# Performance work log

Hardware: AMD Instinct MI355X
Metric: run time of the kernel (lower is better)

## Reference

```python
import jax, jax.numpy as jnp
import numpy as np

N = 100000
E = 3200000
F_IN = 27
H1, C1 = 8, 8
H2, C2 = 1, 2
NEG_SLOPE = 0.2


def gat_conv(x, src, dst, W, a_src, a_dst, b, heads, ch, n_nodes):
    # x: [N, F_in]; src/dst: [E'] (self-loops already appended)
    h = (x @ W).reshape(n_nodes, heads, ch)            # [N, H, C]
    alpha_src = jnp.sum(h * a_src, axis=-1)            # [N, H]
    alpha_dst = jnp.sum(h * a_dst, axis=-1)            # [N, H]
    e = jax.nn.leaky_relu(alpha_src[src] + alpha_dst[dst], NEG_SLOPE)  # [E', H]
    m = jax.ops.segment_max(e, dst, num_segments=n_nodes)             # [N, H]
    ex = jnp.exp(e - m[dst])
    denom = jax.ops.segment_sum(ex, dst, num_segments=n_nodes)        # [N, H]
    alpha = ex / denom[dst]                                           # [E', H]
    out = jax.ops.segment_sum(h[src] * alpha[:, :, None], dst, num_segments=n_nodes)
    return out.reshape(n_nodes, heads * ch) + b


def setup_inputs() -> dict:
    key = jax.random.key(0)
    ks = jax.random.split(key, 10)
    x = jax.random.normal(ks[0], (N, F_IN), dtype=jnp.float32)
    edge_index = jax.random.randint(ks[1], (2, E), 0, N, dtype=jnp.int64)
    s1 = 1.0 / np.sqrt(F_IN)
    s2 = 1.0 / np.sqrt(H1 * C1)
    W1 = jax.random.uniform(ks[2], (F_IN, H1 * C1), jnp.float32, -s1, s1)
    a_src1 = jax.random.uniform(ks[3], (H1, C1), jnp.float32, -s1, s1)
    a_dst1 = jax.random.uniform(ks[4], (H1, C1), jnp.float32, -s1, s1)
    b1 = jnp.zeros((H1 * C1,), jnp.float32)
    W2 = jax.random.uniform(ks[5], (H1 * C1, H2 * C2), jnp.float32, -s2, s2)
    a_src2 = jax.random.uniform(ks[6], (H2, C2), jnp.float32, -s2, s2)
    a_dst2 = jax.random.uniform(ks[7], (H2, C2), jnp.float32, -s2, s2)
    b2 = jnp.zeros((H2 * C2,), jnp.float32)
    return {"x": x, "edge_index": edge_index, "W1": W1, "a_src1": a_src1,
            "a_dst1": a_dst1, "b1": b1, "W2": W2, "a_src2": a_src2,
            "a_dst2": a_dst2, "b2": b2}


def reference(x, edge_index, W1, a_src1, a_dst1, b1, W2, a_src2, a_dst2, b2):
    # eval mode: dropouts are identity. PyG GATConv adds self-loops by default.
    loop = jnp.arange(N, dtype=edge_index.dtype)
    src = jnp.concatenate([edge_index[0], loop])
    dst = jnp.concatenate([edge_index[1], loop])
    h = jax.nn.elu(gat_conv(x, src, dst, W1, a_src1, a_dst1, b1, H1, C1, N))
    out = gat_conv(h, src, dst, W2, a_src2, a_dst2, b2, H2, C2, N)
    return jax.nn.log_softmax(out, axis=1)
```

## Files before the change

kernel.cpp:

```cpp
#include <hip/hip_runtime.h>
#include <hip/hip_fp16.h>
#include <math.h>

#define NN 100000
#define EE 3200000
#define ET (EE + NN)

#define H1n 8
#define C1n 8
#define F1n 64
#define FINn 27
#define NEG 0.2f

#define NPB 128
#define NB 782
#define STRIDE 5120
#define TILE 4096
#define ABLK 256
#define WIN (STRIDE + NPB)
#define FBLK 512
#define RPT 10

typedef float floatx2 __attribute__((ext_vector_type(2)));

static __device__ __forceinline__ float lrelu(float v) {
    return v > 0.f ? v : NEG * v;
}

__global__ __launch_bounds__(ABLK) void k_binA(const int* __restrict__ ei,
                                               int* __restrict__ tail,
                                               int* __restrict__ recs) {
    __shared__ int hist[NB];
    __shared__ int lofs[NB];
    __shared__ int gpos[NB];
    __shared__ int sorted[TILE];
    __shared__ unsigned short sbkt[TILE];
    __shared__ int part[ABLK];

    int tid = threadIdx.x;
    long long e0 = (long long)blockIdx.x * TILE;
    int cnt = (int)min((long long)TILE, (long long)EE - e0);

    for (int i = tid; i < NB; i += ABLK) hist[i] = 0;
    __syncthreads();

    int ss[TILE / ABLK], dd[TILE / ABLK], rk[TILE / ABLK];
    #pragma unroll
    for (int k = 0; k < TILE / ABLK; ++k) {
        int idx = k * ABLK + tid;
        if (idx < cnt) {
            ss[k] = ei[e0 + idx];
            dd[k] = ei[EE + e0 + idx];
            rk[k] = atomicAdd(&hist[dd[k] >> 7], 1);
        }
    }
    __syncthreads();
    {
        const int CH = (NB + ABLK - 1) / ABLK;
        int beg = tid * CH, end = min(beg + CH, NB);
        int s = 0;
        for (int i = beg; i < end; ++i) s += hist[i];
        part[tid] = s;
        __syncthreads();
        for (int off = 1; off < ABLK; off <<= 1) {
            int add = (tid >= off) ? part[tid - off] : 0;
            __syncthreads();
            part[tid] += add;
            __syncthreads();
        }
        int ex = (tid > 0) ? part[tid - 1] : 0;
        for (int i = beg; i < end; ++i) {
            lofs[i] = ex;
            ex += hist[i];
        }
    }
    __syncthreads();
    #pragma unroll
    for (int k = 0; k < TILE / ABLK; ++k) {
        int idx = k * ABLK + tid;
        if (idx < cnt) {
            int b = dd[k] >> 7;
            int r = lofs[b] + rk[k];
            sorted[r] = ss[k] | ((dd[k] & (NPB - 1)) << 17);
            sbkt[r] = (unsigned short)b;
        }
    }
    __syncthreads();
    for (int i = tid; i < NB; i += ABLK) {
        int c = hist[i];
        if (c > 0) gpos[i] = atomicAdd(&tail[i], c);
    }
    __syncthreads();
    for (int t = tid; t < cnt; t += ABLK) {
        int b = sbkt[t];
        recs[(size_t)b * STRIDE + gpos[b] + (t - lofs[b])] = sorted[t];
    }
}

__global__ __launch_bounds__(256) void k_h1(const float* __restrict__ x,
                                            const float* __restrict__ W1,
                                            const float* __restrict__ a_src1,
                                            const float* __restrict__ a_dst1,
                                            unsigned char* __restrict__ h1qA,
                                            unsigned char* __restrict__ h1qB,
                                            __half* __restrict__ as1hA,
                                            __half* __restrict__ as1hB,
                                            float* __restrict__ ad1) {
    int gt = blockIdx.x * blockDim.x + threadIdx.x;
    int n = gt >> 6;
    if (n >= NN) return;
    int lane = threadIdx.x & 63;
    const float* xr = x + (size_t)n * FINn;
    float s = 0.f;
    #pragma unroll
    for (int k = 0; k < FINn; ++k) s = fmaf(xr[k], W1[k * F1n + lane], s);
    float s2 = __shfl_down(s, 1, 64);
    if (!(lane & 1)) {
        int pk = __builtin_amdgcn_cvt_pk_fp8_f32(s, s2, 0, false);
        unsigned char* tb = (lane < 32) ? h1qA : h1qB;
        ((unsigned short*)(tb + (size_t)n * 32))[(lane & 31) >> 1] =
            (unsigned short)(pk & 0xFFFF);
    }
    float ps = s * a_src1[lane];
    float pd = s * a_dst1[lane];
    #pragma unroll
    for (int off = 1; off < 8; off <<= 1) {
        ps += __shfl_xor(ps, off, 64);
        pd += __shfl_xor(pd, off, 64);
    }
    if ((lane & 7) == 0) {
        int h = lane >> 3;
        __half* ta = (h < 4) ? as1hA : as1hB;
        ta[n * 4 + (h & 3)] = __float2half(ps);
        ad1[n * H1n + h] = pd;
    }
}

__global__ __launch_bounds__(FBLK) void k_f1(const int* __restrict__ recs,
                                             const int* __restrict__ tail,
                                             const unsigned* __restrict__ h1qA,
                                             const unsigned* __restrict__ h1qB,
                                             const __half* __restrict__ as1hA,
                                             const __half* __restrict__ as1hB,
                                             const float* __restrict__ ad1,
                                             const float* __restrict__ b1,
                                             const float* __restrict__ W2,
                                             const float* __restrict__ a_src2,
                                             const float* __restrict__ a_dst2,
                                             uint2* __restrict__ rec2,
                                             int* __restrict__ gwin,
                                             uint2* __restrict__ nrange) {
    __shared__ int hist[NPB];
    __shared__ int cur[NPB];
    __shared__ int rloc[NPB + 1];
    __shared__ int window[WIN];
    __shared__ int wtot[2];
    __shared__ float2 part2[NPB];

    int b = blockIdx.x;
    int tid = threadIdx.x;
    int node0 = b * NPB;
    int nodes = min(NPB, NN - node0);
    int rcnt = tail[b];
    const int* rb = recs + (size_t)b * STRIDE;

    if (tid < NPB) hist[tid] = 0;
    __syncthreads();
    int rg[RPT];
    int nmine = 0;
    #pragma unroll
    for (int k = 0; k < RPT; ++k) {
        int i = tid + k * FBLK;
        if (i < rcnt) {
            rg[k] = rb[i];
            atomicAdd(&hist[rg[k] >> 17], 1);
            nmine = k + 1;
        }
    }
    __syncthreads();
    int v = 0, inc = 0;
    if (tid < NPB) {
        v = (tid < nodes) ? hist[tid] + 1 : 0;
        inc = v;
        #pragma unroll
        for (int off = 1; off < 64; off <<= 1) {
            int t = __shfl_up(inc, off, 64);
            if ((tid & 63) >= off) inc += t;
        }
        if ((tid & 63) == 63) wtot[tid >> 6] = inc;
    }
    __syncthreads();
    if (tid < NPB) {
        if (tid >= 64) inc += wtot[0];
        int ex = inc - v;
        if (tid < nodes) {
            rloc[tid] = ex;
            cur[tid] = ex + 1;
            window[ex] = node0 + tid;
        }
    }
    if (tid == 0) rloc[nodes] = wtot[0] + wtot[1];
    __syncthreads();
    #pragma unroll
    for (int k = 0; k < RPT; ++k) {
        if (k < nmine) {
            int r = rg[k];
            int p = atomicAdd(&cur[r >> 17], 1);
            window[p] = r & 0x1FFFF;
        }
    }
    __syncthreads();
    {
        int T = rloc[nodes];
        int gbase = b * WIN;
        for (int i = tid; i < T; i += FBLK)
            gwin[gbase + i] = window[i];
        if (tid < nodes) {
            uint2 r;
            r.x = (unsigned)(gbase + rloc[tid]);
            r.y = (unsigned)(gbase + rloc[tid + 1]);
            nrange[node0 + tid] = r;
        }
    }

    int lane = tid & 63;
    int wv = tid >> 6;
    int hh4 = lane & 3;
    int c4h = lane & 7;
    int bps = lane & 60;
    int bpq = (lane >> 3) << 2;
    int bpx = ((lane >> 3) << 4) + ((c4h >> 1) << 2);

    #pragma unroll
    for (int pass = 0; pass < 2; ++pass) {
        const unsigned* h1h = pass ? h1qB : h1qA;
        const __half* as1h = pass ? as1hB : as1hA;
        int ch0 = pass * 32 + c4h * 4;
        float bch0 = b1[ch0 + 0], bch1 = b1[ch0 + 1];
        float bch2 = b1[ch0 + 2], bch3 = b1[ch0 + 3];
        float w2a0 = W2[(ch0 + 0) * 2], w2b0 = W2[(ch0 + 0) * 2 + 1];
        float w2a1 = W2[(ch0 + 1) * 2], w2b1 = W2[(ch0 + 1) * 2 + 1];
        float w2a2 = W2[(ch0 + 2) * 2], w2b2 = W2[(ch0 + 2) * 2 + 1];
        float w2a3 = W2[(ch0 + 3) * 2], w2b3 = W2[(ch0 + 3) * 2 + 1];

        for (int ln = wv; ln < nodes; ln += FBLK / 64) {
            int n = node0 + ln;
            float adh = ad1[(n << 3) + (pass << 2) + hh4];
            int beg = rloc[ln], end = rloc[ln + 1];
            float a0 = 0.f, a1 = 0.f, a2 = 0.f, a3 = 0.f, den = 0.f;

            for (int base = beg; base < end; base += 64) {
                int cnt = min(64, end - base);
                int sidx = (lane < cnt) ? window[base + lane] : 0;
                for (int sb = 0; sb < cnt; sb += 16) {
                    int sb4 = sb << 2;
                    int s_sc = __builtin_amdgcn_ds_bpermute(sb4 + bps, sidx);
                    float A = __half2float(as1h[((unsigned)s_sc << 2) + hh4]);
                    float sc = A + adh;
                    sc = fmaxf(sc, 0.2f * sc);
                    float x = (sb + (lane >> 2) < cnt) ? __expf(sc) : 0.f;
                    den += x;
                    int xi = __float_as_int(x);
                    #pragma unroll
                    for (int jj = 0; jj < 2; ++jj) {
                        int s_a = __builtin_amdgcn_ds_bpermute(
                            sb4 + (jj << 5) + bpq, sidx);
                        int xr_ = __builtin_amdgcn_ds_bpermute((jj << 7) + bpx, xi);
                        float xv = __int_as_float(xr_);
                        unsigned dw = h1h[((unsigned)s_a << 3) + c4h];
                        floatx2 lo = __builtin_amdgcn_cvt_pk_f32_fp8((int)dw, false);
                        floatx2 hi = __builtin_amdgcn_cvt_pk_f32_fp8((int)dw, true);
                        a0 = fmaf(xv, lo.x, a0);
                        a1 = fmaf(xv, lo.y, a1);
                        a2 = fmaf(xv, hi.x, a2);
                        a3 = fmaf(xv, hi.y, a3);
                    }
                }
            }

            den += __shfl_xor(den, 4, 64);
            den += __shfl_xor(den, 8, 64);
            den += __shfl_xor(den, 16, 64);
            den += __shfl_xor(den, 32, 64);
            den = __int_as_float(__builtin_amdgcn_ds_bpermute(
                (c4h >> 1) << 2, __float_as_int(den)));
            #pragma unroll
            for (int off = 8; off < 64; off <<= 1) {
                a0 += __shfl_xor(a0, off, 64);
                a1 += __shfl_xor(a1, off, 64);
                a2 += __shfl_xor(a2, off, 64);
                a3 += __shfl_xor(a3, off, 64);
            }
            float inv = 1.f / den;
            float v0 = a0 * inv + bch0;
            float v1 = a1 * inv + bch1;
            float v2 = a2 * inv + bch2;
            float v3 = a3 * inv + bch3;
            v0 = v0 > 0.f ? v0 : expm1f(v0);
            v1 = v1 > 0.f ? v1 : expm1f(v1);
            v2 = v2 > 0.f ? v2 : expm1f(v2);
            v3 = v3 > 0.f ? v3 : expm1f(v3);
            float p0 = v0 * w2a0 + v1 * w2a1 + v2 * w2a2 + v3 * w2a3;
            float p1 = v0 * w2b0 + v1 * w2b1 + v2 * w2b2 + v3 * w2b3;
            p0 += __shfl_xor(p0, 1, 64);
            p1 += __shfl_xor(p1, 1, 64);
            p0 += __shfl_xor(p0, 2, 64);
            p1 += __shfl_xor(p1, 2, 64);
            p0 += __shfl_xor(p0, 4, 64);
            p1 += __shfl_xor(p1, 4, 64);
            if (pass == 0) {
                if (lane == 0) part2[ln] = make_float2(p0, p1);
            } else if (lane == 0) {
                float2 pp = part2[ln];
                p0 += pp.x;
                p1 += pp.y;
                float as2 = p0 * a_src2[0] + p1 * a_src2[1];
                float ad2 = p0 * a_dst2[0] + p1 * a_dst2[1];
                __half2 lo2 = __floats2half2_rn(p0, p1);
                __half2 hi2 = __floats2half2_rn(as2, ad2);
                uint2 r;
                r.x = *(unsigned*)&lo2;
                r.y = *(unsigned*)&hi2;
                rec2[n] = r;
            }
        }
    }
}

__global__ __launch_bounds__(256) void k_f2(const int* __restrict__ gwin,
                                            const uint2* __restrict__ nrange,
                                            const uint2* __restrict__ rec2,
                                            const float* __restrict__ b2,
                                            float* __restrict__ out) {
    int n = blockIdx.x * blockDim.x + threadIdx.x;
    if (n >= NN) return;
    __half2 mysd = *(const __half2*)&rec2[n].y;
    float adv = __half2float(__high2half(mysd));
    uint2 rr = nrange[n];
    float den = 0.f, a0 = 0.f, a1 = 0.f;
    for (unsigned i = rr.x; i < rr.y; ++i) {
        int s = gwin[i];
        uint2 rv = rec2[s];
        __half2 h01 = *(const __half2*)&rv.x;
        __half2 hsd = *(const __half2*)&rv.y;
        float e = lrelu(__half2float(__low2half(hsd)) + adv);
        float ex = __expf(e);
        den += ex;
        a0 = fmaf(ex, __half2float(__low2half(h01)), a0);
        a1 = fmaf(ex, __half2float(__high2half(h01)), a1);
    }
    float v0 = a0 / den + b2[0];
    float v1 = a1 / den + b2[1];
    float mx = fmaxf(v0, v1);
    float ls = mx + logf(__expf(v0 - mx) + __expf(v1 - mx));
    float2 o;
    o.x = v0 - ls;
    o.y = v1 - ls;
    ((float2*)out)[n] = o;
}

extern "C" void kernel_launch(void* const* d_in, const int* in_sizes, int n_in,
                              void* d_out, int out_size, void* d_ws, size_t ws_size,
                              hipStream_t stream) {
    const float* x      = (const float*)d_in[0];
    const int*   ei     = (const int*)d_in[1];
    const float* W1     = (const float*)d_in[2];
    const float* a_src1 = (const float*)d_in[3];
    const float* a_dst1 = (const float*)d_in[4];
    const float* b1     = (const float*)d_in[5];
    const float* W2     = (const float*)d_in[6];
    const float* a_src2 = (const float*)d_in[7];
    const float* a_dst2 = (const float*)d_in[8];
    const float* b2     = (const float*)d_in[9];
    float* out = (float*)d_out;

    char* wsb = (char*)d_ws;
    size_t o = 0;
    uint2* rec2 = (uint2*)wsb;                   o += (size_t)NN * 8;
    uint2* nrange = (uint2*)(wsb + o);           o += (size_t)NN * 8;
    #define ALLOC(name, type, count) type* name = (type*)(wsb + o); o += (size_t)(count) * 4;
    ALLOC(ad1,    float, NN * H1n)
    ALLOC(recs,   int,   (size_t)NB * STRIDE)
    ALLOC(gwin,   int,   (size_t)NB * WIN)
    ALLOC(tail,   int,   NB)
    #undef ALLOC
    __half* as1hA = (__half*)(wsb + o);              o += (size_t)NN * 4 * 2;
    __half* as1hB = (__half*)(wsb + o);              o += (size_t)NN * 4 * 2;
    unsigned char* h1qA = (unsigned char*)(wsb + o); o += (size_t)NN * 32;
    unsigned char* h1qB = (unsigned char*)(wsb + o); o += (size_t)NN * 32;

    const int B = 256;
    #define GRID(n) ((unsigned)(((long long)(n) + B - 1) / B))

    hipMemsetAsync(tail, 0, (size_t)NB * sizeof(int), stream);
    k_binA<<<(EE + TILE - 1) / TILE, ABLK, 0, stream>>>(ei, tail, recs);

    k_h1<<<GRID((size_t)NN * 64), B, 0, stream>>>(x, W1, a_src1, a_dst1,
                                                  h1qA, h1qB, as1hA, as1hB, ad1);

    k_f1<<<NB, FBLK, 0, stream>>>(recs, tail, (const unsigned*)h1qA,
                                  (const unsigned*)h1qB, as1hA, as1hB, ad1, b1,
                                  W2, a_src2, a_dst2, rec2, gwin, nrange);

    k_f2<<<GRID(NN), B, 0, stream>>>(gwin, nrange, rec2, b2, out);
    #undef GRID
}
```

Before: 258.1 us.

## Split fused sort+aggregate kernel into sort and per-pass wave-per-node kernels

The fused layer-1 kernel, which sorted bucket records in LDS and then aggregated features, is split in two. A sort-only kernel builds the CSR window and ranges, and two templated kernels (one per head half) each handle one node per wavefront across the whole grid, passing partial layer-2 projections through a global buffer. This is meant to give more parallelism and better load balance than 782 blocks looping over 128 nodes each. The cost is extra launches, re-reading the window from global memory twice, and the extra partial buffer. The binning kernel's block scan also moves from a barrier-heavy LDS scan to a wave shuffle scan with folded offsets.

```diff
diff --git a/kernel.cpp b/kernel.cpp
--- a/kernel.cpp
+++ b/kernel.cpp
@@ -17,6 +17,7 @@
 #define STRIDE 5120
 #define TILE 4096
 #define ABLK 256
+#define EPT (TILE / ABLK)
 #define WIN (STRIDE + NPB)
 #define FBLK 512
 #define RPT 10
@@ -32,10 +33,10 @@
                                                int* __restrict__ recs) {
     __shared__ int hist[NB];
     __shared__ int lofs[NB];
-    __shared__ int gpos[NB];
+    __shared__ int wofs[NB];
     __shared__ int sorted[TILE];
     __shared__ unsigned short sbkt[TILE];
-    __shared__ int part[ABLK];
+    __shared__ int wls[ABLK / 64];
 
     int tid = threadIdx.x;
     long long e0 = (long long)blockIdx.x * TILE;
@@ -44,9 +45,9 @@
     for (int i = tid; i < NB; i += ABLK) hist[i] = 0;
     __syncthreads();
 
-    int ss[TILE / ABLK], dd[TILE / ABLK], rk[TILE / ABLK];
-    #pragma unroll
-    for (int k = 0; k < TILE / ABLK; ++k) {
+    int ss[EPT], dd[EPT], rk[EPT];
+    #pragma unroll
+    for (int k = 0; k < EPT; ++k) {
         int idx = k * ABLK + tid;
         if (idx < cnt) {
             ss[k] = ei[e0 + idx];
@@ -60,15 +61,19 @@
         int beg = tid * CH, end = min(beg + CH, NB);
         int s = 0;
         for (int i = beg; i < end; ++i) s += hist[i];
-        part[tid] = s;
+        int lane = tid & 63, wv = tid >> 6;
+        int inc = s;
+        #pragma unroll
+        for (int off = 1; off < 64; off <<= 1) {
+            int t = __shfl_up(inc, off, 64);
+            if (lane >= off) inc += t;
+        }
+        if (lane == 63) wls[wv] = inc;
         __syncthreads();
-        for (int off = 1; off < ABLK; off <<= 1) {
-            int add = (tid >= off) ? part[tid - off] : 0;
-            __syncthreads();
-            part[tid] += add;
-            __syncthreads();
-        }
-        int ex = (tid > 0) ? part[tid - 1] : 0;
+        int pre = 0;
+        #pragma unroll
+        for (int w = 0; w < ABLK / 64; ++w) pre += (w < wv) ? wls[w] : 0;
+        int ex = pre + inc - s;
         for (int i = beg; i < end; ++i) {
             lofs[i] = ex;
             ex += hist[i];
@@ -76,7 +81,7 @@
     }
     __syncthreads();
     #pragma unroll
-    for (int k = 0; k < TILE / ABLK; ++k) {
+    for (int k = 0; k < EPT; ++k) {
         int idx = k * ABLK + tid;
         if (idx < cnt) {
             int b = dd[k] >> 7;
@@ -88,12 +93,13 @@
     __syncthreads();
     for (int i = tid; i < NB; i += ABLK) {
         int c = hist[i];
-        if (c > 0) gpos[i] = atomicAdd(&tail[i], c);
+        int g = (c > 0) ? atomicAdd(&tail[i], c) : 0;
+        wofs[i] = g - lofs[i];
     }
     __syncthreads();
     for (int t = tid; t < cnt; t += ABLK) {
         int b = sbkt[t];
-        recs[(size_t)b * STRIDE + gpos[b] + (t - lofs[b])] = sorted[t];
+        recs[(size_t)b * STRIDE + wofs[b] + t] = sorted[t];
     }
 }
 
@@ -136,26 +142,15 @@
     }
 }
 
-__global__ __launch_bounds__(FBLK) void k_f1(const int* __restrict__ recs,
-                                             const int* __restrict__ tail,
-                                             const unsigned* __restrict__ h1qA,
-                                             const unsigned* __restrict__ h1qB,
-                                             const __half* __restrict__ as1hA,
-                                             const __half* __restrict__ as1hB,
-                                             const float* __restrict__ ad1,
-                                             const float* __restrict__ b1,
-                                             const float* __restrict__ W2,
-                                             const float* __restrict__ a_src2,
-                                             const float* __restrict__ a_dst2,
-                                             uint2* __restrict__ rec2,
-                                             int* __restrict__ gwin,
-                                             uint2* __restrict__ nrange) {
+__global__ __launch_bounds__(FBLK) void k_sort(const int* __restrict__ recs,
+                                               const int* __restrict__ tail,
+                                               int* __restrict__ gwin,
+                                               uint2* __restrict__ nrange) {
     __shared__ int hist[NPB];
     __shared__ int cur[NPB];
     __shared__ int rloc[NPB + 1];
     __shared__ int window[WIN];
     __shared__ int wtot[2];
-    __shared__ float2 part2[NPB];
 
     int b = blockIdx.x;
     int tid = threadIdx.x;
@@ -210,119 +205,124 @@
         }
     }
     __syncthreads();
-    {
-        int T = rloc[nodes];
-        int gbase = b * WIN;
-        for (int i = tid; i < T; i += FBLK)
-            gwin[gbase + i] = window[i];
-        if (tid < nodes) {
-            uint2 r;
-            r.x = (unsigned)(gbase + rloc[tid]);
-            r.y = (unsigned)(gbase + rloc[tid + 1]);
-            nrange[node0 + tid] = r;
-        }
-    }
-
-    int lane = tid & 63;
-    int wv = tid >> 6;
+    int T = rloc[nodes];
+    int gbase = b * WIN;
+    for (int i = tid; i < T; i += FBLK)
+        gwin[gbase + i] = window[i];
+    if (tid < nodes) {
+        uint2 r;
+        r.x = (unsigned)(gbase + rloc[tid]);
+        r.y = (unsigned)(gbase + rloc[tid + 1]);
+        nrange[node0 + tid] = r;
+    }
+}
+
+template <int PASS>
+__global__ __launch_bounds__(FBLK) void k_mp2(const int* __restrict__ gwin,
+                                              const uint2* __restrict__ nrange,
+                                              const unsigned* __restrict__ h1h,
+                                              const __half* __restrict__ as1h,
+                                              const float* __restrict__ ad1,
+                                              const float* __restrict__ b1,
+                                              const float* __restrict__ W2,
+                                              const float* __restrict__ a_src2,
+                                              const float* __restrict__ a_dst2,
+                                              float2* __restrict__ part,
+                                              uint2* __restrict__ rec2) {
+    int n = (int)(((unsigned)blockIdx.x * FBLK + threadIdx.x) >> 6);
+    if (n >= NN) return;
+    int lane = threadIdx.x & 63;
     int hh4 = lane & 3;
     int c4h = lane & 7;
     int bps = lane & 60;
     int bpq = (lane >> 3) << 2;
     int bpx = ((lane >> 3) << 4) + ((c4h >> 1) << 2);
 
-    #pragma unroll
-    for (int pass = 0; pass < 2; ++pass) {
-        const unsigned* h1h = pass ? h1qB : h1qA;
-        const __half* as1h = pass ? as1hB : as1hA;
-        int ch0 = pass * 32 + c4h * 4;
-        float bch0 = b1[ch0 + 0], bch1 = b1[ch0 + 1];
-        float bch2 = b1[ch0 + 2], bch3 = b1[ch0 + 3];
-        float w2a0 = W2[(ch0 + 0) * 2], w2b0 = W2[(ch0 + 0) * 2 + 1];
-        float w2a1 = W2[(ch0 + 1) * 2], w2b1 = W2[(ch0 + 1) * 2 + 1];
-        float w2a2 = W2[(ch0 + 2) * 2], w2b2 = W2[(ch0 + 2) * 2 + 1];
-        float w2a3 = W2[(ch0 + 3) * 2], w2b3 = W2[(ch0 + 3) * 2 + 1];
-
-        for (int ln = wv; ln < nodes; ln += FBLK / 64) {
-            int n = node0 + ln;
-            float adh = ad1[(n << 3) + (pass << 2) + hh4];
-            int beg = rloc[ln], end = rloc[ln + 1];
-            float a0 = 0.f, a1 = 0.f, a2 = 0.f, a3 = 0.f, den = 0.f;
-
-            for (int base = beg; base < end; base += 64) {
-                int cnt = min(64, end - base);
-                int sidx = (lane < cnt) ? window[base + lane] : 0;
-                for (int sb = 0; sb < cnt; sb += 16) {
-                    int sb4 = sb << 2;
-                    int s_sc = __builtin_amdgcn_ds_bpermute(sb4 + bps, sidx);
-                    float A = __half2float(as1h[((unsigned)s_sc << 2) + hh4]);
-                    float sc = A + adh;
-                    sc = fmaxf(sc, 0.2f * sc);
-                    float x = (sb + (lane >> 2) < cnt) ? __expf(sc) : 0.f;
-                    den += x;
-                    int xi = __float_as_int(x);
-                    #pragma unroll
-                    for (int jj = 0; jj < 2; ++jj) {
-                        int s_a = __builtin_amdgcn_ds_bpermute(
-                            sb4 + (jj << 5) + bpq, sidx);
-                        int xr_ = __builtin_amdgcn_ds_bpermute((jj << 7) + bpx, xi);
-                        float xv = __int_as_float(xr_);
-                        unsigned dw = h1h[((unsigned)s_a << 3) + c4h];
-                        floatx2 lo = __builtin_amdgcn_cvt_pk_f32_fp8((int)dw, false);
-                        floatx2 hi = __builtin_amdgcn_cvt_pk_f32_fp8((int)dw, true);
-                        a0 = fmaf(xv, lo.x, a0);
-                        a1 = fmaf(xv, lo.y, a1);
-                        a2 = fmaf(xv, hi.x, a2);
-                        a3 = fmaf(xv, hi.y, a3);
-                    }
-                }
+    float adh = ad1[(n << 3) + (PASS << 2) + hh4];
+    int ch0 = PASS * 32 + c4h * 4;
+    float bch0 = b1[ch0 + 0], bch1 = b1[ch0 + 1];
+    float bch2 = b1[ch0 + 2], bch3 = b1[ch0 + 3];
+    float w2a0 = W2[(ch0 + 0) * 2], w2b0 = W2[(ch0 + 0) * 2 + 1];
+    float w2a1 = W2[(ch0 + 1) * 2], w2b1 = W2[(ch0 + 1) * 2 + 1];
+    float w2a2 = W2[(ch0 + 2) * 2], w2b2 = W2[(ch0 + 2) * 2 + 1];
+    float w2a3 = W2[(ch0 + 3) * 2], w2b3 = W2[(ch0 + 3) * 2 + 1];
+
+    uint2 rr = nrange[n];
+    float a0 = 0.f, a1 = 0.f, a2 = 0.f, a3 = 0.f, den = 0.f;
+
+    for (unsigned base = rr.x; base < rr.y; base += 64) {
+        int cnt = (int)min(64u, rr.y - base);
+        int sidx = (lane < cnt) ? __builtin_nontemporal_load(&gwin[base + lane]) : 0;
+        for (int sb = 0; sb < cnt; sb += 16) {
+            int sb4 = sb << 2;
+            int s_sc = __builtin_amdgcn_ds_bpermute(sb4 + bps, sidx);
+            float A = __half2float(as1h[((unsigned)s_sc << 2) + hh4]);
+            float sc = A + adh;
+            sc = fmaxf(sc, 0.2f * sc);
+            float x = (sb + (lane >> 2) < cnt) ? __expf(sc) : 0.f;
+            den += x;
+            int xi = __float_as_int(x);
+            #pragma unroll
+            for (int jj = 0; jj < 2; ++jj) {
+                int s_a = __builtin_amdgcn_ds_bpermute(sb4 + (jj << 5) + bpq, sidx);
+                int xr_ = __builtin_amdgcn_ds_bpermute((jj << 7) + bpx, xi);
+                float xv = __int_as_float(xr_);
+                unsigned dw = h1h[((unsigned)s_a << 3) + c4h];
+                floatx2 lo = __builtin_amdgcn_cvt_pk_f32_fp8((int)dw, false);
+                floatx2 hi = __builtin_amdgcn_cvt_pk_f32_fp8((int)dw, true);
+                a0 = fmaf(xv, lo.x, a0);
+                a1 = fmaf(xv, lo.y, a1);
+                a2 = fmaf(xv, hi.x, a2);
+                a3 = fmaf(xv, hi.y, a3);
             }
-
-            den += __shfl_xor(den, 4, 64);
-            den += __shfl_xor(den, 8, 64);
-            den += __shfl_xor(den, 16, 64);
-            den += __shfl_xor(den, 32, 64);
-            den = __int_as_float(__builtin_amdgcn_ds_bpermute(
-                (c4h >> 1) << 2, __float_as_int(den)));
-            #pragma unroll
-            for (int off = 8; off < 64; off <<= 1) {
-                a0 += __shfl_xor(a0, off, 64);
-                a1 += __shfl_xor(a1, off, 64);
-                a2 += __shfl_xor(a2, off, 64);
-                a3 += __shfl_xor(a3, off, 64);
-            }
-            float inv = 1.f / den;
-            float v0 = a0 * inv + bch0;
-            float v1 = a1 * inv + bch1;
-            float v2 = a2 * inv + bch2;
-            float v3 = a3 * inv + bch3;
-            v0 = v0 > 0.f ? v0 : expm1f(v0);
-            v1 = v1 > 0.f ? v1 : expm1f(v1);
-            v2 = v2 > 0.f ? v2 : expm1f(v2);
-            v3 = v3 > 0.f ? v3 : expm1f(v3);
-            float p0 = v0 * w2a0 + v1 * w2a1 + v2 * w2a2 + v3 * w2a3;
-            float p1 = v0 * w2b0 + v1 * w2b1 + v2 * w2b2 + v3 * w2b3;
-            p0 += __shfl_xor(p0, 1, 64);
-            p1 += __shfl_xor(p1, 1, 64);
-            p0 += __shfl_xor(p0, 2, 64);
-            p1 += __shfl_xor(p1, 2, 64);
-            p0 += __shfl_xor(p0, 4, 64);
-            p1 += __shfl_xor(p1, 4, 64);
-            if (pass == 0) {
-                if (lane == 0) part2[ln] = make_float2(p0, p1);
-            } else if (lane == 0) {
-                float2 pp = part2[ln];
-                p0 += pp.x;
-                p1 += pp.y;
-                float as2 = p0 * a_src2[0] + p1 * a_src2[1];
-                float ad2 = p0 * a_dst2[0] + p1 * a_dst2[1];
-                __half2 lo2 = __floats2half2_rn(p0, p1);
-                __half2 hi2 = __floats2half2_rn(as2, ad2);
-                uint2 r;
-                r.x = *(unsigned*)&lo2;
-                r.y = *(unsigned*)&hi2;
-                rec2[n] = r;
-            }
+        }
+    }
+
+    den += __shfl_xor(den, 4, 64);
+    den += __shfl_xor(den, 8, 64);
+    den += __shfl_xor(den, 16, 64);
+    den += __shfl_xor(den, 32, 64);
+    den = __int_as_float(
+        __builtin_amdgcn_ds_bpermute((c4h >> 1) << 2, __float_as_int(den)));
+    #pragma unroll
+    for (int off = 8; off < 64; off <<= 1) {
+        a0 += __shfl_xor(a0, off, 64);
+        a1 += __shfl_xor(a1, off, 64);
+        a2 += __shfl_xor(a2, off, 64);
+        a3 += __shfl_xor(a3, off, 64);
+    }
+    float inv = 1.f / den;
+    float v0 = a0 * inv + bch0;
+    float v1 = a1 * inv + bch1;
+    float v2 = a2 * inv + bch2;
+    float v3 = a3 * inv + bch3;
+    v0 = v0 > 0.f ? v0 : expm1f(v0);
+    v1 = v1 > 0.f ? v1 : expm1f(v1);
+    v2 = v2 > 0.f ? v2 : expm1f(v2);
+    v3 = v3 > 0.f ? v3 : expm1f(v3);
+    float p0 = v0 * w2a0 + v1 * w2a1 + v2 * w2a2 + v3 * w2a3;
+    float p1 = v0 * w2b0 + v1 * w2b1 + v2 * w2b2 + v3 * w2b3;
+    p0 += __shfl_xor(p0, 1, 64);
+    p1 += __shfl_xor(p1, 1, 64);
+    p0 += __shfl_xor(p0, 2, 64);
+    p1 += __shfl_xor(p1, 2, 64);
+    p0 += __shfl_xor(p0, 4, 64);
+    p1 += __shfl_xor(p1, 4, 64);
+    if (lane == 0) {
+        if (PASS == 0) {
+            part[n] = make_float2(p0, p1);
+        } else {
+            float2 pp = part[n];
+            p0 += pp.x;
+            p1 += pp.y;
+            float as2 = p0 * a_src2[0] + p1 * a_src2[1];
+            float ad2 = p0 * a_dst2[0] + p1 * a_dst2[1];
+            __half2 lo2 = __floats2half2_rn(p0, p1);
+            __half2 hi2 = __floats2half2_rn(as2, ad2);
+            uint2 r;
+            r.x = *(unsigned*)&lo2;
+            r.y = *(unsigned*)&hi2;
+            rec2[n] = r;
         }
     }
 }
@@ -378,6 +378,7 @@
     size_t o = 0;
     uint2* rec2 = (uint2*)wsb;                   o += (size_t)NN * 8;
     uint2* nrange = (uint2*)(wsb + o);           o += (size_t)NN * 8;
+    float2* part = (float2*)(wsb + o);           o += (size_t)NN * 8;
     #define ALLOC(name, type, count) type* name = (type*)(wsb + o); o += (size_t)(count) * 4;
     ALLOC(ad1,    float, NN * H1n)
     ALLOC(recs,   int,   (size_t)NB * STRIDE)
@@ -398,9 +399,13 @@
     k_h1<<<GRID((size_t)NN * 64), B, 0, stream>>>(x, W1, a_src1, a_dst1,
                                                   h1qA, h1qB, as1hA, as1hB, ad1);
 
-    k_f1<<<NB, FBLK, 0, stream>>>(recs, tail, (const unsigned*)h1qA,
-                                  (const unsigned*)h1qB, as1hA, as1hB, ad1, b1,
-                                  W2, a_src2, a_dst2, rec2, gwin, nrange);
+    k_sort<<<NB, FBLK, 0, stream>>>(recs, tail, gwin, nrange);
+
+    unsigned mpg = (unsigned)(((size_t)NN * 64 + FBLK - 1) / FBLK);
+    k_mp2<0><<<mpg, FBLK, 0, stream>>>(gwin, nrange, (const unsigned*)h1qA, as1hA,
+                                       ad1, b1, W2, a_src2, a_dst2, part, rec2);
+    k_mp2<1><<<mpg, FBLK, 0, stream>>>(gwin, nrange, (const unsigned*)h1qB, as1hB,
+                                       ad1, b1, W2, a_src2, a_dst2, part, rec2);
 
     k_f2<<<GRID(NN), B, 0, stream>>>(gwin, nrange, rec2, b2, out);
     #undef GRID
```

After: 252.6 us. -2.2%, faster.
